# Optimization experiments

Measured on AMD Instinct MI355X. Metric: run time of the kernel, lower is better.

Reference implementation:

```python
import jax, jax.numpy as jnp
import numpy as np
from math import factorial as fact

# openmx, nao_max=14: row = col = 1x0e+1x0e+1x0e+1x1o+1x1o+1x2e (dim 14)
NAO = 14
LS = [0, 0, 0, 1, 1, 2]
IDX_CHANGE = np.array([0, 1, 2, 5, 3, 4, 8, 6, 7, 11, 13, 9, 12, 10])
IDX_INV = np.empty(NAO, dtype=np.int64)
IDX_INV[IDX_CHANGE] = np.arange(NAO)


def _su2_cg(j1, m1, j2, m2, j3, m3):
    # SU(2) Clebsch-Gordan coefficient <j1 m1 j2 m2 | j3 m3> (Racah formula, e3nn convention)
    if m3 != m1 + m2:
        return 0.0
    vmin = max(-j1 + j2 + m3, -j1 + m1, 0)
    vmax = min(j2 + j3 + m1, j3 - j1 + j2, j3 + m3)
    c = ((2 * j3 + 1) * fact(j3 + j1 - j2) * fact(j3 - j1 + j2) * fact(j1 + j2 - j3)
         * fact(j3 + m3) * fact(j3 - m3)
         / (fact(j1 + j2 + j3 + 1) * fact(j1 - m1) * fact(j1 + m1)
            * fact(j2 - m2) * fact(j2 + m2))) ** 0.5
    s = 0.0
    for v in range(vmin, vmax + 1):
        s += (-1) ** (v + j2 + m2) * fact(j2 + j3 + m1 - v) * fact(j1 - m1 + v) / (
            fact(v) * fact(j3 - j1 + j2 - v) * fact(j3 + m3 - v) * fact(v + j1 - j2 - m3))
    return c * s


def _q_real_to_complex(l):
    # change of basis real spherical harmonics -> complex (e3nn convention, incl. (-i)^l phase)
    q = np.zeros((2 * l + 1, 2 * l + 1), dtype=np.complex128)
    for m in range(-l, 0):
        q[l + m, l + abs(m)] = 1 / 2 ** 0.5
        q[l + m, l - abs(m)] = -1j / 2 ** 0.5
    q[l, l] = 1
    for m in range(1, l + 1):
        q[l + m, l + abs(m)] = (-1) ** m / 2 ** 0.5
        q[l + m, l - abs(m)] = 1j * (-1) ** m / 2 ** 0.5
    return (-1j) ** l * q


def wigner_3j(l1, l2, l3):
    # real-basis Wigner 3j tensor (norm 1), shape (2l1+1, 2l2+1, 2l3+1)
    csu2 = np.zeros((2 * l1 + 1, 2 * l2 + 1, 2 * l3 + 1))
    for m1 in range(-l1, l1 + 1):
        for m2 in range(-l2, l2 + 1):
            m3 = m1 + m2
            if -l3 <= m3 <= l3:
                csu2[l1 + m1, l2 + m2, l3 + m3] = _su2_cg(l1, m1, l2, m2, l3, m3)
    q1, q2, q3 = _q_real_to_complex(l1), _q_real_to_complex(l2), _q_real_to_complex(l3)
    cc = np.einsum('ia,kb,nc,ikn->abc', q1, q2, np.conj(q3), csu2)
    c = cc.real if np.linalg.norm(cc.real) >= np.linalg.norm(cc.imag) else cc.imag
    return c / np.linalg.norm(c)


def _build_blocks():
    # enumerate all (li, lj, L) blocks in source order and compute sorted-irreps permutation
    blocks = []   # (row_start, n_rows, col_start, n_cols, cg[2L+1, 2li+1, 2lj+1])
    irreps = []   # (L, parity) of each output block
    rs = 0
    for li in LS:
        nr = 2 * li + 1
        cs = 0
        for lj in LS:
            nc = 2 * lj + 1
            for L in range(abs(li - lj), li + lj + 1):
                blocks.append((rs, nr, cs, nc, wigner_3j(L, li, lj)))
                irreps.append((L, (-1) ** (li + lj)))
            cs += nc
        rs += nr
    # e3nn Irreps.sort: stable sort by (l, parity); inv[k] = original index of k-th sorted block
    inv_perm = sorted(range(len(irreps)), key=lambda i: irreps[i])
    return blocks, inv_perm

BLOCKS, INV_PERM = _build_blocks()


def setup_inputs() -> dict:
    key = jax.random.key(0)
    x = jax.random.normal(key, (500000, NAO, NAO), dtype=jnp.float32)
    return {"x": x}


def reference(x):
    x = x.reshape(-1, NAO, NAO)
    # _change_index_inv: openmx has no minus_index (double negation cancels), only inverse permute
    x = x[:, IDX_INV[:, None], IDX_INV[None, :]]
    outs = []
    for rs, nr, cs, nc, cg in BLOCKS:
        blk = x[:, rs:rs + nr, cs:cs + nc]              # [N, 2li+1, 2lj+1]
        outs.append(jnp.einsum('nij,kij->nk', blk, jnp.asarray(cg, x.dtype)))
    return jnp.concatenate([outs[i] for i in INV_PERM], axis=-1)  # [N, 196]
```

## Files before the change

### kernel.cpp

```cpp
#include <hip/hip_runtime.h>
#include <utility>

#define NAO   14
#define NOUT  196
#define NBLK  56
#define TS    64
#define ROWP  197
#define MAXW  28
#define NTHR  512


struct Meta { int L, li, lj, rs, cs, off; };
constexpr Meta META[NBLK] = {
  {0,0,0,0,0,0},{0,0,0,0,1,1},{0,0,0,0,2,2},{1,0,1,0,3,14},{1,0,1,0,6,17},{2,0,2,0,9,97},
  {0,0,0,1,0,3},{0,0,0,1,1,4},{0,0,0,1,2,5},{1,0,1,1,3,20},{1,0,1,1,6,23},{2,0,2,1,9,102},
  {0,0,0,2,0,6},{0,0,0,2,1,7},{0,0,0,2,2,8},{1,0,1,2,3,26},{1,0,1,2,6,29},{2,0,2,2,9,107},
  {1,1,0,3,0,32},{1,1,0,3,1,35},{1,1,0,3,2,38},
  {0,1,1,3,3,9},{1,1,1,3,3,62},{2,1,1,3,3,112},
  {0,1,1,3,6,10},{1,1,1,3,6,65},{2,1,1,3,6,117},
  {1,1,2,3,9,41},{2,1,2,3,9,77},{3,1,2,3,9,152},
  {1,1,0,6,0,44},{1,1,0,6,1,47},{1,1,0,6,2,50},
  {0,1,1,6,3,11},{1,1,1,6,3,68},{2,1,1,6,3,122},
  {0,1,1,6,6,12},{1,1,1,6,6,71},{2,1,1,6,6,127},
  {1,1,2,6,9,53},{2,1,2,6,9,82},{3,1,2,6,9,159},
  {2,2,0,9,0,132},{2,2,0,9,1,137},{2,2,0,9,2,142},
  {1,2,1,9,3,56},{2,2,1,9,3,87},{3,2,1,9,3,166},
  {1,2,1,9,6,59},{2,2,1,9,6,92},{3,2,1,9,6,173},
  {0,2,2,9,9,13},{1,2,2,9,9,74},{2,2,2,9,9,147},{3,2,2,9,9,180},{4,2,2,9,9,187}
};
constexpr int IDXINV[NAO] = {0,1,2,4,5,3,7,8,6,11,13,9,12,10};

constexpr double cfact(int n){ double r=1.0; for (int i=2;i<=n;++i) r*=(double)i; return r; }
constexpr double csqrt(double x){
  if (x<=0.0) return 0.0;
  double g = x>1.0 ? x : 1.0;
  for (int i=0;i<200;++i){ double ng = 0.5*(g + x/g); if (ng==g) break; g=ng; }
  return g;
}

constexpr double su2_cg(int j1,int m1,int j2,int m2,int j3,int m3){
  if (m3 != m1+m2) return 0.0;
  int vmin = -j1+j2+m3; if (-j1+m1>vmin) vmin=-j1+m1; if (0>vmin) vmin=0;
  int vmax = j2+j3+m1;  if (j3-j1+j2<vmax) vmax=j3-j1+j2; if (j3+m3<vmax) vmax=j3+m3;
  if (vmax < vmin) return 0.0;
  double c = csqrt((2.0*j3+1.0)*cfact(j3+j1-j2)*cfact(j3-j1+j2)*cfact(j1+j2-j3)*
                   cfact(j3+m3)*cfact(j3-m3) /
                   (cfact(j1+j2+j3+1)*cfact(j1-m1)*cfact(j1+m1)*cfact(j2-m2)*cfact(j2+m2)));
  double s = 0.0;
  for (int v=vmin; v<=vmax; ++v){
    double t = cfact(j2+j3+m1-v)*cfact(j1-m1+v) /
               (cfact(v)*cfact(j3-j1+j2-v)*cfact(j3+m3-v)*cfact(v+j1-j2-m3));
    s += (((v+j2+m2)&1) ? -1.0 : 1.0) * t;
  }
  return c*s;
}

struct QMat { double re[81]; double im[81]; };
constexpr QMat build_q(int l){
  QMat q{};
  int n = 2*l+1;
  const double is2 = 0.70710678118654752440;
  for (int m=-l; m<0; ++m){ q.re[(l+m)*n+(l-m)] = is2; q.im[(l+m)*n+(l+m)] = -is2; }
  q.re[l*n+l] = 1.0;
  for (int m=1; m<=l; ++m){
    double sgn = (m&1) ? -1.0 : 1.0;
    q.re[(l+m)*n+(l+m)] = sgn*is2;
    q.im[(l+m)*n+(l-m)] = sgn*is2;
  }
  int ph = l & 3;
  if (ph){
    for (int t=0; t<n*n; ++t){
      double a=q.re[t], b=q.im[t];
      if (ph==1)      { q.re[t]= b; q.im[t]=-a; }
      else if (ph==2) { q.re[t]=-a; q.im[t]=-b; }
      else            { q.re[t]=-b; q.im[t]= a; }
    }
  }
  return q;
}

struct BlockCG { double v[225]; };
constexpr BlockCG build_block_cg(int L,int li,int lj){
  int n1=2*L+1, n2=2*li+1, n3=2*lj+1;
  double csu2[225] = {};
  for (int i=0;i<n1;++i)
    for (int k=0;k<n2;++k){
      int m1=i-L, m2=k-li, m3=m1+m2;
      if (m3>=-lj && m3<=lj)
        csu2[(i*n2+k)*n3 + (m3+lj)] = su2_cg(L,m1,li,m2,lj,m3);
    }
  QMat q1 = build_q(L), q2 = build_q(li), q3 = build_q(lj);
  double ccr[225] = {}, cci[225] = {};
  double re2=0.0, im2=0.0;
  for (int a=0;a<n1;++a)
    for (int b=0;b<n2;++b)
      for (int c=0;c<n3;++c){
        double accr=0.0, acci=0.0;
        for (int i=0;i<n1;++i){
          double ar=q1.re[i*n1+a], ai=q1.im[i*n1+a];
          if (ar==0.0 && ai==0.0) continue;
          for (int k=0;k<n2;++k){
            double br=q2.re[k*n2+b], bi=q2.im[k*n2+b];
            if (br==0.0 && bi==0.0) continue;
            double pr=ar*br-ai*bi, pi=ar*bi+ai*br;
            for (int n=0;n<n3;++n){
              double w = csu2[(i*n2+k)*n3+n];
              if (w==0.0) continue;
              double cr = q3.re[n*n3+c], ci = -q3.im[n*n3+c];
              accr += w*(pr*cr - pi*ci);
              acci += w*(pr*ci + pi*cr);
            }
          }
        }
        ccr[(a*n2+b)*n3+c]=accr; cci[(a*n2+b)*n3+c]=acci;
        re2 += accr*accr; im2 += acci*acci;
      }
  BlockCG out{};
  bool pick_re = csqrt(re2) >= csqrt(im2);
  double inv = 1.0 / csqrt(pick_re ? re2 : im2);
  for (int t=0; t<n1*n2*n3; ++t) out.v[t] = (pick_re ? ccr[t] : cci[t]) * inv;
  return out;
}

template<int B> struct BlockV {
  static constexpr BlockCG cg = build_block_cg(META[B].L, META[B].li, META[B].lj);
};

constexpr int tau_map(int a){ return (3*a) % 49; }
constexpr int sig_map(int c){ return 4*tau_map(c>>2) + (c&3); }

struct Tables {
  int   nnz[NOUT];
  int   cols[NOUT][MAXW];
  float wts[NOUT][MAXW];
  bool  ok;
};

template<int... Bs>
constexpr Tables build_tables_impl(std::integer_sequence<int,Bs...>){
  const BlockCG cgs[NBLK] = { BlockV<Bs>::cg... };
  Tables t{};
  bool seen[NOUT] = {};
  t.ok = true;
  for (int b=0; b<NBLK; ++b){
    int n1=2*META[b].L+1, n2=2*META[b].li+1, n3=2*META[b].lj+1;
    for (int k=0; k<n1; ++k){
      int p = META[b].off + k;
      if (p < 0 || p >= NOUT || seen[p]) { t.ok = false; continue; }
      seen[p] = true;
      int q = 0;
      for (int i=0;i<n2;++i)
        for (int j=0;j<n3;++j){
          double v = cgs[b].v[(k*n2+i)*n3+j];
          if (v > 1e-10 || v < -1e-10){
            if (q >= MAXW) { t.ok = false; continue; }
            int col = IDXINV[META[b].rs+i]*NAO + IDXINV[META[b].cs+j];
            if (col < 0 || col >= NOUT) t.ok = false;
            t.cols[p][q] = sig_map(col);
            t.wts[p][q]  = (float)v;
            ++q;
          }
        }
      t.nnz[p] = q;
    }
  }
  for (int p=0;p<NOUT;++p) if (!seen[p] || t.nnz[p] < 1) t.ok = false;
  return t;
}
constexpr Tables TBL = build_tables_impl(std::make_integer_sequence<int,NBLK>{});
static_assert(TBL.ok, "Wigner CSR table build failed consistency checks");

constexpr int NWAVE = 8;
constexpr int WBEG[NWAVE+1] = {0,56,77,94,128,154,171,185,196};


template<int P>
__device__ __forceinline__ float dot_row(const float* row){
  float acc = 0.f;
  #pragma unroll
  for (int q = 0; q < TBL.nnz[P]; ++q)
    acc = fmaf(TBL.wts[P][q], row[TBL.cols[P][q]], acc);
  return acc;
}

template<int W, int... I>
__device__ __forceinline__ void wave_compute_impl(const float* row, float* acc,
                                                  std::integer_sequence<int,I...>){
  ((acc[I] = dot_row<WBEG[W]+I>(row)), ...);
}
template<int W>
__device__ __forceinline__ void wave_compute(const float* row, float* acc){
  wave_compute_impl<W>(row, acc,
      std::make_integer_sequence<int, WBEG[W+1]-WBEG[W]>{});
}

template<int W, int... I>
__device__ __forceinline__ void wave_store_impl(float* xrow, const float* acc,
                                                std::integer_sequence<int,I...>){
  ((xrow[sig_map(WBEG[W]+I)] = acc[I]), ...);
}
template<int W>
__device__ __forceinline__ void wave_store(float* xrow, const float* acc){
  wave_store_impl<W>(xrow, acc,
      std::make_integer_sequence<int, WBEG[W+1]-WBEG[W]>{});
}

__device__ __forceinline__ int tau_rt(int a){
  int t3 = 3*a;
  t3 -= (t3 >= 98) ? 98 : ((t3 >= 49) ? 49 : 0);
  return t3;
}

__global__ __launch_bounds__(NTHR, 4)
void expand_kernel(const float* __restrict__ x, float* __restrict__ out, int total){
  __shared__ float xs[TS*ROWP];

  const int tid  = threadIdx.x;
  const int lane = tid & 63;
  const int wid  = tid >> 6;
  const int base = blockIdx.x * (TS*NOUT);

  for (int t4 = tid; t4 < TS*49; t4 += NTHR){
    int g = base + 4*t4;
    float4 v = make_float4(0.f,0.f,0.f,0.f);
    if (g < total) v = ((const float4*)x)[(base>>2) + t4];
    int s = t4/49, a = t4 - 49*s;
    float* w = &xs[s*ROWP + 4*tau_rt(a)];
    w[0]=v.x; w[1]=v.y; w[2]=v.z; w[3]=v.w;
  }
  __syncthreads();

  const float* row = &xs[lane*ROWP];
  float acc[56];
  switch (wid){
    case 0: wave_compute<0>(row, acc); break;
    case 1: wave_compute<1>(row, acc); break;
    case 2: wave_compute<2>(row, acc); break;
    case 3: wave_compute<3>(row, acc); break;
    case 4: wave_compute<4>(row, acc); break;
    case 5: wave_compute<5>(row, acc); break;
    case 6: wave_compute<6>(row, acc); break;
    default: wave_compute<7>(row, acc); break;
  }
  __syncthreads();

  float* xrow = &xs[lane*ROWP];
  switch (wid){
    case 0: wave_store<0>(xrow, acc); break;
    case 1: wave_store<1>(xrow, acc); break;
    case 2: wave_store<2>(xrow, acc); break;
    case 3: wave_store<3>(xrow, acc); break;
    case 4: wave_store<4>(xrow, acc); break;
    case 5: wave_store<5>(xrow, acc); break;
    case 6: wave_store<6>(xrow, acc); break;
    default: wave_store<7>(xrow, acc); break;
  }
  __syncthreads();

  for (int t4 = tid; t4 < TS*49; t4 += NTHR){
    int gf = base + 4*t4;
    if (gf >= total) break;
    int s = t4/49, a = t4 - 49*s;
    const float* o = &xs[s*ROWP + 4*tau_rt(a)];
    float4 v; v.x=o[0]; v.y=o[1]; v.z=o[2]; v.w=o[3];
    *(float4*)&out[gf] = v;
  }
}

extern "C" void kernel_launch(void* const* d_in, const int* in_sizes, int n_in,
                              void* d_out, int out_size, void* d_ws, size_t ws_size,
                              hipStream_t stream) {
  const float* x = (const float*)d_in[0];
  float* out = (float*)d_out;
  int total   = in_sizes[0];
  int nsamp   = total / NOUT;
  int nblocks = (nsamp + TS - 1) / TS;
  expand_kernel<<<dim3(nblocks), dim3(NTHR), 0, stream>>>(x, out, total);
}
```

Before: 618.8 us.

## Use persistent workgroups with register prefetch of next tile and nontemporal stores

```diff
diff --git a/kernel.cpp b/kernel.cpp
--- a/kernel.cpp
+++ b/kernel.cpp
@@ -8,6 +8,9 @@
 #define ROWP  197
 #define MAXW  28
 #define NTHR  512
+#define NPWG  512
+
+typedef float vf4 __attribute__((ext_vector_type(4)));
 
 
 struct Meta { int L, li, lj, rs, cs, off; };
@@ -218,52 +221,90 @@
   const int tid  = threadIdx.x;
   const int lane = tid & 63;
   const int wid  = tid >> 6;
-  const int base = blockIdx.x * (TS*NOUT);
-
-  for (int t4 = tid; t4 < TS*49; t4 += NTHR){
-    int g = base + 4*t4;
-    float4 v = make_float4(0.f,0.f,0.f,0.f);
-    if (g < total) v = ((const float4*)x)[(base>>2) + t4];
-    int s = t4/49, a = t4 - 49*s;
-    float* w = &xs[s*ROWP + 4*tau_rt(a)];
-    w[0]=v.x; w[1]=v.y; w[2]=v.z; w[3]=v.w;
-  }
-  __syncthreads();
-
-  const float* row = &xs[lane*ROWP];
-  float acc[56];
-  switch (wid){
-    case 0: wave_compute<0>(row, acc); break;
-    case 1: wave_compute<1>(row, acc); break;
-    case 2: wave_compute<2>(row, acc); break;
-    case 3: wave_compute<3>(row, acc); break;
-    case 4: wave_compute<4>(row, acc); break;
-    case 5: wave_compute<5>(row, acc); break;
-    case 6: wave_compute<6>(row, acc); break;
-    default: wave_compute<7>(row, acc); break;
-  }
-  __syncthreads();
-
-  float* xrow = &xs[lane*ROWP];
-  switch (wid){
-    case 0: wave_store<0>(xrow, acc); break;
-    case 1: wave_store<1>(xrow, acc); break;
-    case 2: wave_store<2>(xrow, acc); break;
-    case 3: wave_store<3>(xrow, acc); break;
-    case 4: wave_store<4>(xrow, acc); break;
-    case 5: wave_store<5>(xrow, acc); break;
-    case 6: wave_store<6>(xrow, acc); break;
-    default: wave_store<7>(xrow, acc); break;
-  }
-  __syncthreads();
-
-  for (int t4 = tid; t4 < TS*49; t4 += NTHR){
-    int gf = base + 4*t4;
-    if (gf >= total) break;
-    int s = t4/49, a = t4 - 49*s;
-    const float* o = &xs[s*ROWP + 4*tau_rt(a)];
-    float4 v; v.x=o[0]; v.y=o[1]; v.z=o[2]; v.w=o[3];
-    *(float4*)&out[gf] = v;
+  const int ntiles = (total + TS*NOUT - 1) / (TS*NOUT);
+
+  int tile = blockIdx.x;
+  if (tile >= ntiles) return;
+
+  vf4 pf[7];
+  #pragma unroll
+  for (int u = 0; u < 7; ++u){
+    int t4 = tid + NTHR*u;
+    int g  = tile*(TS*NOUT) + 4*t4;
+    pf[u] = (vf4)(0.f);
+    if (t4 < TS*49 && g < total)
+      pf[u] = ((const vf4*)x)[tile*(TS*49) + t4];
+  }
+
+  for (;;){
+    const int base = tile*(TS*NOUT);
+
+    #pragma unroll
+    for (int u = 0; u < 7; ++u){
+      int t4 = tid + NTHR*u;
+      if (t4 < TS*49){
+        int s = t4/49, a = t4 - 49*s;
+        float* w = &xs[s*ROWP + 4*tau_rt(a)];
+        w[0]=pf[u].x; w[1]=pf[u].y; w[2]=pf[u].z; w[3]=pf[u].w;
+      }
+    }
+    __syncthreads();
+
+    const float* row = &xs[lane*ROWP];
+    float acc[56];
+    switch (wid){
+      case 0: wave_compute<0>(row, acc); break;
+      case 1: wave_compute<1>(row, acc); break;
+      case 2: wave_compute<2>(row, acc); break;
+      case 3: wave_compute<3>(row, acc); break;
+      case 4: wave_compute<4>(row, acc); break;
+      case 5: wave_compute<5>(row, acc); break;
+      case 6: wave_compute<6>(row, acc); break;
+      default: wave_compute<7>(row, acc); break;
+    }
+    __syncthreads();
+
+    float* xrow = &xs[lane*ROWP];
+    switch (wid){
+      case 0: wave_store<0>(xrow, acc); break;
+      case 1: wave_store<1>(xrow, acc); break;
+      case 2: wave_store<2>(xrow, acc); break;
+      case 3: wave_store<3>(xrow, acc); break;
+      case 4: wave_store<4>(xrow, acc); break;
+      case 5: wave_store<5>(xrow, acc); break;
+      case 6: wave_store<6>(xrow, acc); break;
+      default: wave_store<7>(xrow, acc); break;
+    }
+
+    const int ntile = tile + NPWG;
+    if (ntile < ntiles){
+      #pragma unroll
+      for (int u = 0; u < 7; ++u){
+        int t4 = tid + NTHR*u;
+        int g  = ntile*(TS*NOUT) + 4*t4;
+        if (t4 < TS*49 && g < total)
+          pf[u] = ((const vf4*)x)[ntile*(TS*49) + t4];
+      }
+    }
+    __syncthreads();
+
+    #pragma unroll
+    for (int u = 0; u < 7; ++u){
+      int t4 = tid + NTHR*u;
+      if (t4 < TS*49){
+        int gf = base + 4*t4;
+        if (gf < total){
+          int s = t4/49, a = t4 - 49*s;
+          const float* o = &xs[s*ROWP + 4*tau_rt(a)];
+          vf4 v; v.x=o[0]; v.y=o[1]; v.z=o[2]; v.w=o[3];
+          __builtin_nontemporal_store(v, (vf4*)&out[gf]);
+        }
+      }
+    }
+
+    if (ntile >= ntiles) break;
+    tile = ntile;
+    __syncthreads();
   }
 }
 
@@ -274,6 +315,7 @@
   float* out = (float*)d_out;
   int total   = in_sizes[0];
   int nsamp   = total / NOUT;
-  int nblocks = (nsamp + TS - 1) / TS;
+  int ntiles  = (nsamp + TS - 1) / TS;
+  int nblocks = ntiles < NPWG ? ntiles : NPWG;
   expand_kernel<<<dim3(nblocks), dim3(NTHR), 0, stream>>>(x, out, total);
 }
```

Measured after the change: 641.9 us. +3.7%, slower.
